# Optimization experiments

Hardware: AMD Instinct MI355X
Metric: run time of the kernel (lower is better)

The kernel has to match this reference:

```python
import jax, jax.numpy as jnp
import numpy as np

N, E = 50000, 400000
HID, HT = 128, 128
HEADS, C = 4, 128  # TransformerConv heads=4, out_channels=hidden_X


def setup_inputs() -> dict:
    key = jax.random.key(0)
    ks = jax.random.split(key, 16)
    s = lambda k, shape, fan: jax.random.normal(k, shape, jnp.float32) / np.sqrt(fan)
    return {
        "edge_index": jax.random.randint(ks[0], (2, E), 0, N, dtype=jnp.int32),
        "h_X": jax.random.normal(ks[1], (N, HID), jnp.float32),
        "h_t": jax.random.normal(ks[2], (1, HT), jnp.float32),
        # TransformerConv params: lin_query/key/value: (HID -> HEADS*C), lin_skip: (HID -> C)
        "Wq": s(ks[3], (HID, HEADS * C), HID), "bq": jnp.zeros((HEADS * C,), jnp.float32),
        "Wk": s(ks[4], (HID, HEADS * C), HID), "bk": jnp.zeros((HEADS * C,), jnp.float32),
        "Wv": s(ks[5], (HID, HEADS * C), HID), "bv": jnp.zeros((HEADS * C,), jnp.float32),
        "Wskip": s(ks[6], (HID, C), HID), "bskip": jnp.zeros((C,), jnp.float32),
        # update_X: Linear(HID+HT -> HID), LayerNorm(HID)
        "Wup": s(ks[7], (HID + HT, HID), HID + HT), "bup": jnp.zeros((HID,), jnp.float32),
        "gamma": jnp.ones((HID,), jnp.float32), "beta": jnp.zeros((HID,), jnp.float32),
    }


def transformer_conv(h_X, edge_index, Wq, bq, Wk, bk, Wv, bv, Wskip, bskip):
    n = h_X.shape[0]
    src, dst = edge_index[0], edge_index[1]  # messages flow src -> dst
    q = (h_X @ Wq + bq).reshape(n, HEADS, C)
    k = (h_X @ Wk + bk).reshape(n, HEADS, C)
    v = (h_X @ Wv + bv).reshape(n, HEADS, C)
    # per-edge attention scores [E, H]
    score = jnp.einsum('ehc,ehc->eh', q[dst], k[src]) / np.sqrt(C)
    # segment softmax over incoming edges of each destination node
    m = jax.ops.segment_max(score, dst, num_segments=n)          # [N, H]
    ex = jnp.exp(score - m[dst])                                 # [E, H]
    denom = jax.ops.segment_sum(ex, dst, num_segments=n)        # [N, H]
    alpha = ex / denom[dst]                                      # [E, H]
    agg = jax.ops.segment_sum(alpha[..., None] * v[src], dst, num_segments=n)  # [N, H, C]
    out = agg.mean(axis=1)                                       # concat=False -> mean over heads
    return out + h_X @ Wskip + bskip                             # root_weight=True


def reference(edge_index, h_X, h_t, Wq, bq, Wk, bk, Wv, bv, Wskip, bskip,
              Wup, bup, gamma, beta):
    n = h_X.shape[0]
    h_att = transformer_conv(h_X, edge_index, Wq, bq, Wk, bk, Wv, bv, Wskip, bskip)
    h_t_exp = jnp.broadcast_to(h_t, (n, h_t.shape[1]))
    h = jnp.concatenate([h_att, h_t_exp], axis=1)
    h = jax.nn.relu(h @ Wup + bup)
    # LayerNorm (eps=1e-5); Dropout is identity in eval
    mu = h.mean(axis=-1, keepdims=True)
    var = ((h - mu) ** 2).mean(axis=-1, keepdims=True)
    return (h - mu) / jnp.sqrt(var + 1e-5) * gamma + beta
```

## Files before the change

### kernel.cpp

```cpp
#include <hip/hip_runtime.h>

typedef unsigned short u16;
typedef unsigned int   u32;

#define HID   128
#define HEADS 4
#define CH    128
#define HC    512
#define KVW   1024
#define UT    32

typedef __bf16 bf16x8v __attribute__((ext_vector_type(8)));
typedef float  f32x4v  __attribute__((ext_vector_type(4)));
union FragU { uint4 u; bf16x8v b; };

static __device__ __forceinline__ float bf2f(u16 u) {
  union { u32 u; float f; } x;
  x.u = ((u32)u) << 16;
  return x.f;
}
static __device__ __forceinline__ u16 f2bf(float f) {
  union { float f; u32 u; } x;
  x.f = f;
  u32 r = x.u + 0x7fffu + ((x.u >> 16) & 1u);
  return (u16)(r >> 16);
}

static __device__ __forceinline__ void unpack8(uint4 raw, float* dst) {
  dst[0] = bf2f((u16)(raw.x & 0xffffu));
  dst[1] = bf2f((u16)(raw.x >> 16));
  dst[2] = bf2f((u16)(raw.y & 0xffffu));
  dst[3] = bf2f((u16)(raw.y >> 16));
  dst[4] = bf2f((u16)(raw.z & 0xffffu));
  dst[5] = bf2f((u16)(raw.z >> 16));
  dst[6] = bf2f((u16)(raw.w & 0xffffu));
  dst[7] = bf2f((u16)(raw.w >> 16));
}

__global__ void hist_kernel(const int* dst_idx, int* deg, int E) {
  int e = blockIdx.x * 256 + threadIdx.x;
  if (e < E) atomicAdd(&deg[dst_idx[e]], 1);
}

__global__ void blocksum_kernel(const int* deg, int* bsums, int n) {
  __shared__ int buf[256];
  int i = blockIdx.x * 256 + threadIdx.x;
  int v = 0;
  if (i < n) v = deg[i];
  buf[threadIdx.x] = v;
  __syncthreads();
  for (int off = 128; off > 0; off >>= 1) {
    if (threadIdx.x < off) buf[threadIdx.x] += buf[threadIdx.x + off];
    __syncthreads();
  }
  if (threadIdx.x == 0) bsums[blockIdx.x] = buf[0];
}

__global__ void scanb_kernel(const int* bsums, int* boffs, int nb) {
  __shared__ int buf[256];
  __shared__ int carry_s;
  int tid = threadIdx.x;
  if (tid == 0) carry_s = 0;
  __syncthreads();
  for (int base = 0; base < nb; base += 256) {
    int i = base + tid;
    int v = 0;
    if (i < nb) v = bsums[i];
    buf[tid] = v;
    __syncthreads();
    for (int off = 1; off < 256; off <<= 1) {
      int t = 0;
      if (tid >= off) t = buf[tid - off];
      __syncthreads();
      buf[tid] += t;
      __syncthreads();
    }
    int incl = buf[tid] + carry_s;
    if (i < nb) boffs[i] = incl - v;
    __syncthreads();
    if (tid == 255) carry_s = incl;
    __syncthreads();
  }
}

__global__ void scanfinal_kernel(const int* deg, const int* boffs,
                                 int* row_ptr, int* cursor, int n) {
  __shared__ int buf[256];
  int tid = threadIdx.x;
  int i = blockIdx.x * 256 + tid;
  int v = 0;
  if (i < n) v = deg[i];
  buf[tid] = v;
  __syncthreads();
  for (int off = 1; off < 256; off <<= 1) {
    int t = 0;
    if (tid >= off) t = buf[tid - off];
    __syncthreads();
    buf[tid] += t;
    __syncthreads();
  }
  int incl = buf[tid] + boffs[blockIdx.x];
  if (i < n) {
    row_ptr[i + 1] = incl;
    cursor[i] = incl - v;
  }
  if (i == 0) row_ptr[0] = 0;
}

__global__ void scatter_kernel(const int* src_idx, const int* dst_idx,
                               int* cursor, int* col, int E) {
  int e = blockIdx.x * 256 + threadIdx.x;
  if (e < E) {
    int pos = atomicAdd(&cursor[dst_idx[e]], 1);
    col[pos] = src_idx[e];
  }
}

__global__ void packH_kernel(const float* __restrict__ hX,
                             u16* __restrict__ hpack, int N, int total) {
  int i = blockIdx.x * 256 + threadIdx.x;
  if (i >= total) return;
  int j = i & 7;
  int lane = (i >> 3) & 63;
  int kc = (i >> 9) & 3;
  int ntile = i >> 11;
  int node = ntile * 16 + (lane & 15);
  int k = kc * 32 + (lane >> 4) * 8 + j;
  float v = (node < N) ? hX[(size_t)node * HID + k] : 0.f;
  hpack[i] = f2bf(v);
}

__global__ void packW4_kernel(const float* __restrict__ Wq,
                              const float* __restrict__ Wk,
                              const float* __restrict__ Wv,
                              const float* __restrict__ Wsk,
                              u16* __restrict__ Wp, int total) {
  int i = blockIdx.x * 256 + threadIdx.x;
  if (i >= total) return;
  int j = i & 7;
  int lane = (i >> 3) & 63;
  int kc = (i >> 9) & 3;
  int ct = i >> 11;
  int n = ct * 16 + (lane & 15);
  int k = kc * 32 + (lane >> 4) * 8 + j;
  float w;
  if (n < 512) w = Wq[(size_t)k * HC + n];
  else if (n < 1024) w = Wk[(size_t)k * HC + (n - 512)];
  else if (n < 1536) w = Wv[(size_t)k * HC + (n - 1024)];
  else w = Wsk[(size_t)k * HID + (n - 1536)];
  Wp[i] = f2bf(w);
}

__global__ __launch_bounds__(256) void mfma_proj_kernel(
    const u16* __restrict__ hpack, const u16* __restrict__ Wp,
    const float* __restrict__ bq, const float* __restrict__ bk,
    const float* __restrict__ bv, const float* __restrict__ bsk,
    u16* __restrict__ qb, u16* __restrict__ kvb,
    float* __restrict__ skipf, int N) {
  int t = threadIdx.x;
  int wv = t >> 6;
  int L = t & 63;
  int bx = blockIdx.x;
  int my0 = blockIdx.y * 8;

  FragU Bf[2][4];
  const u16* wb0 = Wp + (size_t)(bx * 8 + wv * 2) * 2048;
#pragma unroll
  for (int cc = 0; cc < 2; ++cc)
#pragma unroll
    for (int kc = 0; kc < 4; ++kc)
      Bf[cc][kc].u = *(const uint4*)(wb0 + cc * 2048 + kc * 512 + L * 8);

  int colq = L & 15;
  int quad = L >> 4;
  u16* outB_[2];
  int stride_[2];
  float bval[2];
  int nl_[2];
  int isF32_[2];
#pragma unroll
  for (int cc = 0; cc < 2; ++cc) {
    int n = (bx * 8 + wv * 2 + cc) * 16 + colq;
    const float* bias;
    if (n < 512) {
      outB_[cc] = qb; bias = bq; nl_[cc] = n; stride_[cc] = HC; isF32_[cc] = 0;
    } else if (n < 1024) {
      outB_[cc] = kvb; bias = bk; nl_[cc] = n - 512; stride_[cc] = KVW;
      isF32_[cc] = 0;
    } else if (n < 1536) {
      outB_[cc] = kvb; bias = bv; nl_[cc] = n - 512; stride_[cc] = KVW;
      isF32_[cc] = 0;
    } else {
      outB_[cc] = (u16*)skipf; bias = bsk; nl_[cc] = n - 1536; stride_[cc] = 0;
      isF32_[cc] = 1;
    }
    bval[cc] = bias[nl_[cc]];
  }

  const u16* ha = hpack + (size_t)my0 * 2048;

  for (int mt = 0; mt < 8; mt += 2) {
    FragU a0[4], a1[4];
#pragma unroll
    for (int kc = 0; kc < 4; ++kc) {
      a0[kc].u = *(const uint4*)(ha + (size_t)mt * 2048 + kc * 512 + L * 8);
      a1[kc].u =
          *(const uint4*)(ha + (size_t)(mt + 1) * 2048 + kc * 512 + L * 8);
    }

    f32x4v ac00 = (f32x4v){0.f, 0.f, 0.f, 0.f};
    f32x4v ac01 = (f32x4v){0.f, 0.f, 0.f, 0.f};
    f32x4v ac10 = (f32x4v){0.f, 0.f, 0.f, 0.f};
    f32x4v ac11 = (f32x4v){0.f, 0.f, 0.f, 0.f};
#pragma unroll
    for (int kc = 0; kc < 4; ++kc) {
      ac00 = __builtin_amdgcn_mfma_f32_16x16x32_bf16(a0[kc].b, Bf[0][kc].b,
                                                     ac00, 0, 0, 0);
      ac01 = __builtin_amdgcn_mfma_f32_16x16x32_bf16(a0[kc].b, Bf[1][kc].b,
                                                     ac01, 0, 0, 0);
      ac10 = __builtin_amdgcn_mfma_f32_16x16x32_bf16(a1[kc].b, Bf[0][kc].b,
                                                     ac10, 0, 0, 0);
      ac11 = __builtin_amdgcn_mfma_f32_16x16x32_bf16(a1[kc].b, Bf[1][kc].b,
                                                     ac11, 0, 0, 0);
    }

#pragma unroll
    for (int half = 0; half < 2; ++half) {
      int nodeBase = (my0 + mt + half) * 16 + quad * 4;
#pragma unroll
      for (int cc = 0; cc < 2; ++cc) {
        const f32x4v& a =
            half ? (cc ? ac11 : ac10) : (cc ? ac01 : ac00);
        if (isF32_[cc]) {
#pragma unroll
          for (int rg = 0; rg < 4; ++rg) {
            int node = nodeBase + rg;
            if (node < N)
              skipf[(size_t)node * HID + nl_[cc]] = a[rg] + bval[cc];
          }
        } else {
          u16* ob = outB_[cc];
          int st = stride_[cc];
#pragma unroll
          for (int rg = 0; rg < 4; ++rg) {
            int node = nodeBase + rg;
            if (node < N)
              ob[(size_t)node * st + nl_[cc]] = f2bf(a[rg] + bval[cc]);
          }
        }
      }
    }
  }
}

__global__ void fused_attn_kernel(const u16* __restrict__ qb,
                                  const u16* __restrict__ kvb,
                                  const int* __restrict__ row_ptr,
                                  const int* __restrict__ col_src,
                                  float* out, int N) {
  int node = blockIdx.x * 4 + (threadIdx.x >> 6);
  if (node >= N) return;
  int lane = threadIdx.x & 63;
  int head = lane >> 4;
  int r = lane & 15;
  int foff = head * CH + r * 8;
  const float sscale = 0.08838834764831845f;

  float qf[8];
  unpack8(*(const uint4*)(qb + (size_t)node * HC + foff), qf);

  float m = -3.402823466e38f;
  float l = 0.f;
  float acc[8];
  for (int j = 0; j < 8; ++j) acc[j] = 0.f;

  int e0 = row_ptr[node];
  int e1 = row_ptr[node + 1];
  int e = e0;

  for (; e + 4 <= e1; e += 4) {
    int s0 = col_src[e];
    int s1 = col_src[e + 1];
    int s2 = col_src[e + 2];
    int s3 = col_src[e + 3];
    const u16* r0p = kvb + (size_t)s0 * KVW + foff;
    const u16* r1p = kvb + (size_t)s1 * KVW + foff;
    const u16* r2p = kvb + (size_t)s2 * KVW + foff;
    const u16* r3p = kvb + (size_t)s3 * KVW + foff;
    uint4 k0 = *(const uint4*)(r0p);
    uint4 k1 = *(const uint4*)(r1p);
    uint4 k2 = *(const uint4*)(r2p);
    uint4 k3 = *(const uint4*)(r3p);
    uint4 v0 = *(const uint4*)(r0p + 512);
    uint4 v1 = *(const uint4*)(r1p + 512);
    uint4 v2 = *(const uint4*)(r2p + 512);
    uint4 v3 = *(const uint4*)(r3p + 512);

    float kf0[8], kf1[8], kf2[8], kf3[8];
    unpack8(k0, kf0);
    unpack8(k1, kf1);
    unpack8(k2, kf2);
    unpack8(k3, kf3);
    float p0 = 0.f, p1 = 0.f, p2 = 0.f, p3 = 0.f;
    for (int j = 0; j < 8; ++j) {
      p0 = fmaf(kf0[j], qf[j], p0);
      p1 = fmaf(kf1[j], qf[j], p1);
      p2 = fmaf(kf2[j], qf[j], p2);
      p3 = fmaf(kf3[j], qf[j], p3);
    }
    p0 += __shfl_xor(p0, 1);
    p1 += __shfl_xor(p1, 1);
    p2 += __shfl_xor(p2, 1);
    p3 += __shfl_xor(p3, 1);
    p0 += __shfl_xor(p0, 2);
    p1 += __shfl_xor(p1, 2);
    p2 += __shfl_xor(p2, 2);
    p3 += __shfl_xor(p3, 2);
    p0 += __shfl_xor(p0, 4);
    p1 += __shfl_xor(p1, 4);
    p2 += __shfl_xor(p2, 4);
    p3 += __shfl_xor(p3, 4);
    p0 += __shfl_xor(p0, 8);
    p1 += __shfl_xor(p1, 8);
    p2 += __shfl_xor(p2, 8);
    p3 += __shfl_xor(p3, 8);
    float sc0 = p0 * sscale;
    float sc1 = p1 * sscale;
    float sc2 = p2 * sscale;
    float sc3 = p3 * sscale;
    float mnew = fmaxf(fmaxf(m, fmaxf(sc0, sc1)), fmaxf(sc2, sc3));
    float so = __expf(m - mnew);
    float pe0 = __expf(sc0 - mnew);
    float pe1 = __expf(sc1 - mnew);
    float pe2 = __expf(sc2 - mnew);
    float pe3 = __expf(sc3 - mnew);
    l = l * so + (pe0 + pe1) + (pe2 + pe3);
    float vf0[8], vf1[8], vf2[8], vf3[8];
    unpack8(v0, vf0);
    unpack8(v1, vf1);
    unpack8(v2, vf2);
    unpack8(v3, vf3);
    for (int j = 0; j < 8; ++j) {
      float add = fmaf(pe0, vf0[j],
                       fmaf(pe1, vf1[j], fmaf(pe2, vf2[j], pe3 * vf3[j])));
      acc[j] = fmaf(acc[j], so, add);
    }
    m = mnew;
  }

  for (; e < e1; ++e) {
    int s0 = col_src[e];
    const u16* r0p = kvb + (size_t)s0 * KVW + foff;
    uint4 k0 = *(const uint4*)(r0p);
    uint4 v0 = *(const uint4*)(r0p + 512);
    float kf0[8];
    unpack8(k0, kf0);
    float p0 = 0.f;
    for (int j = 0; j < 8; ++j) p0 = fmaf(kf0[j], qf[j], p0);
    p0 += __shfl_xor(p0, 1);
    p0 += __shfl_xor(p0, 2);
    p0 += __shfl_xor(p0, 4);
    p0 += __shfl_xor(p0, 8);
    float sc0 = p0 * sscale;
    float mnew = fmaxf(m, sc0);
    float so = __expf(m - mnew);
    float pe0 = __expf(sc0 - mnew);
    l = l * so + pe0;
    float vf0[8];
    unpack8(v0, vf0);
    for (int j = 0; j < 8; ++j) acc[j] = fmaf(acc[j], so, pe0 * vf0[j]);
    m = mnew;
  }

  float inv = 0.f;
  if (l > 0.f) inv = 1.0f / l;
  float val[8];
  for (int j = 0; j < 8; ++j) {
    float x = acc[j] * inv;
    x += __shfl_xor(x, 16);
    x += __shfl_xor(x, 32);
    val[j] = x * 0.25f;
  }

  if (head == 0) {
    float* p = out + (size_t)node * HID + r * 8;
    float4 a = *(const float4*)(p);
    float4 b = *(const float4*)(p + 4);
    a.x += val[0]; a.y += val[1]; a.z += val[2]; a.w += val[3];
    b.x += val[4]; b.y += val[5]; b.z += val[6]; b.w += val[7];
    *(float4*)(p) = a;
    *(float4*)(p + 4) = b;
  }
}

__global__ void cvec_kernel(const float* h_t, const float* Wup,
                            const float* bup, float* cvec) {
  __shared__ float part[4][128];
  int c = threadIdx.x & 127;
  int kc = threadIdx.x >> 7;
  float acc = 0.f;
  for (int k = kc * 32; k < kc * 32 + 32; ++k)
    acc = fmaf(h_t[k], Wup[(size_t)(128 + k) * 128 + c], acc);
  part[kc][c] = acc;
  __syncthreads();
  if (kc == 0)
    cvec[c] = part[0][c] + part[1][c] + part[2][c] + part[3][c] + bup[c];
}

__global__ __launch_bounds__(256) void ATTLayer_19396072308956_kernel(
    float* out, const float* __restrict__ Wup, const float* __restrict__ cvec,
    const float* __restrict__ gamma, const float* __restrict__ beta, int N) {
  __shared__ float Wl[64 * 128];
  __shared__ float Hl[UT * 128];
  int t = threadIdx.x;
  int n0 = blockIdx.x * UT;

  for (int i = t * 4; i < UT * 128; i += 1024) {
    int node = n0 + (i >> 7);
    float4 v;
    if (node < N) {
      v = *(const float4*)(out + (size_t)node * HID + (i & 127));
    } else {
      v.x = 0.f; v.y = 0.f; v.z = 0.f; v.w = 0.f;
    }
    *(float4*)(Hl + i) = v;
  }

  int wv = t >> 6;
  int r = t & 63;
  int c0 = 2 * r;
  float2 cv = *(const float2*)(cvec + c0);
  float a0[8];
  float a1[8];
  for (int j = 0; j < 8; ++j) {
    a0[j] = cv.x;
    a1[j] = cv.y;
  }

  for (int ph = 0; ph < 2; ++ph) {
    __syncthreads();
    for (int i = t * 4; i < 64 * 128; i += 1024) {
      *(float4*)(Wl + i) = *(const float4*)(Wup + (size_t)ph * 64 * 128 + i);
    }
    __syncthreads();
    const float* hbase = Hl + (wv * 8) * 128 + ph * 64;
#pragma unroll 8
    for (int k = 0; k < 64; ++k) {
      float2 w2 = *(const float2*)(Wl + k * 128 + c0);
      for (int j = 0; j < 8; ++j) {
        float h = hbase[j * 128 + k];
        a0[j] = fmaf(h, w2.x, a0[j]);
        a1[j] = fmaf(h, w2.y, a1[j]);
      }
    }
  }

  float2 g = *(const float2*)(gamma + c0);
  float2 b = *(const float2*)(beta + c0);
  for (int j = 0; j < 8; ++j) {
    int node = n0 + wv * 8 + j;
    float r0 = fmaxf(a0[j], 0.f);
    float r1 = fmaxf(a1[j], 0.f);
    float s = r0 + r1;
    for (int msk = 1; msk < 64; msk <<= 1) s += __shfl_xor(s, msk);
    float mean = s * (1.0f / 128.0f);
    float d0 = r0 - mean;
    float d1 = r1 - mean;
    float sq = d0 * d0 + d1 * d1;
    for (int msk = 1; msk < 64; msk <<= 1) sq += __shfl_xor(sq, msk);
    float rstd = rsqrtf(sq * (1.0f / 128.0f) + 1e-5f);
    if (node < N) {
      float2 o;
      o.x = d0 * rstd * g.x + b.x;
      o.y = d1 * rstd * g.y + b.y;
      *(float2*)(out + (size_t)node * HID + c0) = o;
    }
  }
}

extern "C" void kernel_launch(void* const* d_in, const int* in_sizes, int n_in,
                              void* d_out, int out_size, void* d_ws,
                              size_t ws_size, hipStream_t stream) {
  (void)n_in;
  (void)out_size;
  (void)ws_size;

  const int* edge_index = (const int*)d_in[0];
  const float* hX    = (const float*)d_in[1];
  const float* h_t   = (const float*)d_in[2];
  const float* Wq    = (const float*)d_in[3];
  const float* bq    = (const float*)d_in[4];
  const float* Wk    = (const float*)d_in[5];
  const float* bk    = (const float*)d_in[6];
  const float* Wv    = (const float*)d_in[7];
  const float* bv    = (const float*)d_in[8];
  const float* Wskip = (const float*)d_in[9];
  const float* bskip = (const float*)d_in[10];
  const float* Wup   = (const float*)d_in[11];
  const float* bup   = (const float*)d_in[12];
  const float* gamma = (const float*)d_in[13];
  const float* beta  = (const float*)d_in[14];

  const int E = in_sizes[0] / 2;
  const int N = in_sizes[1] / HID;
  const int* src_idx = edge_index;
  const int* dst_idx = edge_index + E;
  const int NB = (N + 255) / 256;
  const int NTILES = (N + 15) / 16;
  const int NTILES8 = ((NTILES + 7) / 8) * 8;

  char* w = (char*)d_ws;
  size_t off = 0;
  float* cvec = (float*)(w + off);
  off += 256 * 4;
  int* deg = (int*)(w + off);
  off += ((size_t)N * 4 + 255) / 256 * 256;
  int* row_ptr = (int*)(w + off);
  off += ((size_t)(N + 1) * 4 + 255) / 256 * 256;
  int* cursor = (int*)(w + off);
  off += ((size_t)N * 4 + 255) / 256 * 256;
  int* bsums = (int*)(w + off);
  off += ((size_t)NB * 4 + 255) / 256 * 256;
  int* boffs = (int*)(w + off);
  off += ((size_t)NB * 4 + 255) / 256 * 256;
  int* col = (int*)(w + off);
  off += ((size_t)E * 4 + 255) / 256 * 256;
  u16* hpack = (u16*)(w + off);
  off += ((size_t)NTILES8 * 2048 * 2 + 255) / 256 * 256;
  u16* Wp = (u16*)(w + off);
  off += ((size_t)128 * 1664 * 2 + 255) / 256 * 256;
  u16* bigA = (u16*)(w + off);
  off += ((size_t)N * HC * 2 + 255) / 256 * 256;
  u16* bigKV = (u16*)(w + off);
  off += ((size_t)N * KVW * 2 + 255) / 256 * 256;

  float* out = (float*)d_out;

  hipMemsetAsync(deg, 0, (size_t)N * 4, stream);
  hist_kernel<<<(E + 255) / 256, 256, 0, stream>>>(dst_idx, deg, E);
  blocksum_kernel<<<NB, 256, 0, stream>>>(deg, bsums, N);
  scanb_kernel<<<1, 256, 0, stream>>>(bsums, boffs, NB);
  scanfinal_kernel<<<NB, 256, 0, stream>>>(deg, boffs, row_ptr, cursor, N);
  scatter_kernel<<<(E + 255) / 256, 256, 0, stream>>>(src_idx, dst_idx, cursor,
                                                      col, E);

  int totH = NTILES8 * 2048;
  packH_kernel<<<(totH + 255) / 256, 256, 0, stream>>>(hX, hpack, N, totH);
  packW4_kernel<<<(128 * 1664 + 255) / 256, 256, 0, stream>>>(
      Wq, Wk, Wv, Wskip, Wp, 128 * 1664);

  cvec_kernel<<<1, 512, 0, stream>>>(h_t, Wup, bup, cvec);

  mfma_proj_kernel<<<dim3(13, NTILES8 / 8), 256, 0, stream>>>(
      hpack, Wp, bq, bk, bv, bskip, bigA, bigKV, out, N);

  fused_attn_kernel<<<(N + 3) / 4, 256, 0, stream>>>(bigA, bigKV, row_ptr,
                                                     col, out, N);

  ATTLayer_19396072308956_kernel<<<(N + UT - 1) / UT, 256, 0, stream>>>(
      out, Wup, cvec, gamma, beta, N);
}
```

Baseline: 390.0 us.

## Fuse update linear, ReLU and LayerNorm into attention kernel epilogue

Removes the separate update/LayerNorm kernel and runs the Wup matmul, ReLU and LayerNorm in the epilogue of the attention kernel. Each wave stages its node's aggregated row in shared memory, then each lane computes two output channels by streaming Wup from global memory. This saves one launch and a write/read round trip of the intermediate rows. In exchange, Wup is no longer reused across 32 nodes through shared memory, so every wave re-reads the 64KB weight from cache. A block barrier is also added after the attention loop, which can stall waves with short neighbor lists.

```diff
diff --git a/kernel.cpp b/kernel.cpp
--- a/kernel.cpp
+++ b/kernel.cpp
@@ -8,7 +8,6 @@
 #define CH    128
 #define HC    512
 #define KVW   1024
-#define UT    32
 
 typedef __bf16 bf16x8v __attribute__((ext_vector_type(8)));
 typedef float  f32x4v  __attribute__((ext_vector_type(4)));
@@ -257,25 +256,34 @@
                                   const u16* __restrict__ kvb,
                                   const int* __restrict__ row_ptr,
                                   const int* __restrict__ col_src,
-                                  float* out, int N) {
-  int node = blockIdx.x * 4 + (threadIdx.x >> 6);
-  if (node >= N) return;
+                                  float* out,
+                                  const float* __restrict__ Wup,
+                                  const float* __restrict__ cvec,
+                                  const float* __restrict__ gamma,
+                                  const float* __restrict__ beta, int N) {
+  __shared__ float Hs[4][128];
+  int wv = threadIdx.x >> 6;
+  int node = blockIdx.x * 4 + wv;
   int lane = threadIdx.x & 63;
   int head = lane >> 4;
   int r = lane & 15;
   int foff = head * CH + r * 8;
   const float sscale = 0.08838834764831845f;
+  bool valid = (node < N);
 
   float qf[8];
-  unpack8(*(const uint4*)(qb + (size_t)node * HC + foff), qf);
+  if (valid) unpack8(*(const uint4*)(qb + (size_t)node * HC + foff), qf);
 
   float m = -3.402823466e38f;
   float l = 0.f;
   float acc[8];
   for (int j = 0; j < 8; ++j) acc[j] = 0.f;
 
-  int e0 = row_ptr[node];
-  int e1 = row_ptr[node + 1];
+  int e0 = 0, e1 = 0;
+  if (valid) {
+    e0 = row_ptr[node];
+    e1 = row_ptr[node + 1];
+  }
   int e = e0;
 
   for (; e + 4 <= e1; e += 4) {
@@ -382,14 +390,50 @@
     val[j] = x * 0.25f;
   }
 
-  if (head == 0) {
-    float* p = out + (size_t)node * HID + r * 8;
-    float4 a = *(const float4*)(p);
-    float4 b = *(const float4*)(p + 4);
-    a.x += val[0]; a.y += val[1]; a.z += val[2]; a.w += val[3];
-    b.x += val[4]; b.y += val[5]; b.z += val[6]; b.w += val[7];
-    *(float4*)(p) = a;
-    *(float4*)(p + 4) = b;
+  if (valid && head == 0) {
+    const float* srow = out + (size_t)node * HID + r * 8;
+    float4 a = *(const float4*)(srow);
+    float4 b = *(const float4*)(srow + 4);
+    float* hd = &Hs[wv][r * 8];
+    hd[0] = a.x + val[0];
+    hd[1] = a.y + val[1];
+    hd[2] = a.z + val[2];
+    hd[3] = a.w + val[3];
+    hd[4] = b.x + val[4];
+    hd[5] = b.y + val[5];
+    hd[6] = b.z + val[6];
+    hd[7] = b.w + val[7];
+  }
+  __syncthreads();
+
+  int c0 = lane * 2;
+  float a0 = cvec[c0];
+  float a1 = cvec[c0 + 1];
+  const float* hrow = Hs[wv];
+#pragma unroll 8
+  for (int k = 0; k < 128; ++k) {
+    float hk = hrow[k];
+    float2 w2 = *(const float2*)(Wup + (size_t)k * HID + c0);
+    a0 = fmaf(hk, w2.x, a0);
+    a1 = fmaf(hk, w2.y, a1);
+  }
+  float r0 = fmaxf(a0, 0.f);
+  float r1 = fmaxf(a1, 0.f);
+  float s = r0 + r1;
+  for (int msk = 1; msk < 64; msk <<= 1) s += __shfl_xor(s, msk);
+  float mean = s * (1.0f / 128.0f);
+  float d0 = r0 - mean;
+  float d1 = r1 - mean;
+  float sq = d0 * d0 + d1 * d1;
+  for (int msk = 1; msk < 64; msk <<= 1) sq += __shfl_xor(sq, msk);
+  float rstd = rsqrtf(sq * (1.0f / 128.0f) + 1e-5f);
+  if (valid) {
+    float2 g = *(const float2*)(gamma + c0);
+    float2 b = *(const float2*)(beta + c0);
+    float2 o;
+    o.x = d0 * rstd * g.x + b.x;
+    o.y = d1 * rstd * g.y + b.y;
+    *(float2*)(out + (size_t)node * HID + c0) = o;
   }
 }
 
@@ -405,77 +449,6 @@
   __syncthreads();
   if (kc == 0)
     cvec[c] = part[0][c] + part[1][c] + part[2][c] + part[3][c] + bup[c];
-}
-
-__global__ __launch_bounds__(256) void ATTLayer_19396072308956_kernel(
-    float* out, const float* __restrict__ Wup, const float* __restrict__ cvec,
-    const float* __restrict__ gamma, const float* __restrict__ beta, int N) {
-  __shared__ float Wl[64 * 128];
-  __shared__ float Hl[UT * 128];
-  int t = threadIdx.x;
-  int n0 = blockIdx.x * UT;
-
-  for (int i = t * 4; i < UT * 128; i += 1024) {
-    int node = n0 + (i >> 7);
-    float4 v;
-    if (node < N) {
-      v = *(const float4*)(out + (size_t)node * HID + (i & 127));
-    } else {
-      v.x = 0.f; v.y = 0.f; v.z = 0.f; v.w = 0.f;
-    }
-    *(float4*)(Hl + i) = v;
-  }
-
-  int wv = t >> 6;
-  int r = t & 63;
-  int c0 = 2 * r;
-  float2 cv = *(const float2*)(cvec + c0);
-  float a0[8];
-  float a1[8];
-  for (int j = 0; j < 8; ++j) {
-    a0[j] = cv.x;
-    a1[j] = cv.y;
-  }
-
-  for (int ph = 0; ph < 2; ++ph) {
-    __syncthreads();
-    for (int i = t * 4; i < 64 * 128; i += 1024) {
-      *(float4*)(Wl + i) = *(const float4*)(Wup + (size_t)ph * 64 * 128 + i);
-    }
-    __syncthreads();
-    const float* hbase = Hl + (wv * 8) * 128 + ph * 64;
-#pragma unroll 8
-    for (int k = 0; k < 64; ++k) {
-      float2 w2 = *(const float2*)(Wl + k * 128 + c0);
-      for (int j = 0; j < 8; ++j) {
-        float h = hbase[j * 128 + k];
-        a0[j] = fmaf(h, w2.x, a0[j]);
-        a1[j] = fmaf(h, w2.y, a1[j]);
-      }
-    }
-  }
-
-  float2 g = *(const float2*)(gamma + c0);
-  float2 b = *(const float2*)(beta + c0);
-  for (int j = 0; j < 8; ++j) {
-    int node = n0 + wv * 8 + j;
-    float r0 = fmaxf(a0[j], 0.f);
-    float r1 = fmaxf(a1[j], 0.f);
-    float s = r0 + r1;
-    for (int msk = 1; msk < 64; msk <<= 1) s += __shfl_xor(s, msk);
-    float mean = s * (1.0f / 128.0f);
-    float d0 = r0 - mean;
-    float d1 = r1 - mean;
-    float sq = d0 * d0 + d1 * d1;
-    for (int msk = 1; msk < 64; msk <<= 1) sq += __shfl_xor(sq, msk);
-    float rstd = rsqrtf(sq * (1.0f / 128.0f) + 1e-5f);
-    if (node < N) {
-      float2 o;
-      o.x = d0 * rstd * g.x + b.x;
-      o.y = d1 * rstd * g.y + b.y;
-      *(float2*)(out + (size_t)node * HID + c0) = o;
-    }
-  }
 }
 
 extern "C" void kernel_launch(void* const* d_in, const int* in_sizes, int n_in,
@@ -554,9 +527,6 @@
   mfma_proj_kernel<<<dim3(13, NTILES8 / 8), 256, 0, stream>>>(
       hpack, Wp, bq, bk, bv, bskip, bigA, bigKV, out, N);
 
-  fused_attn_kernel<<<(N + 3) / 4, 256, 0, stream>>>(bigA, bigKV, row_ptr,
-                                                     col, out, N);
-
-  ATTLayer_19396072308956_kernel<<<(N + UT - 1) / UT, 256, 0, stream>>>(
-      out, Wup, cvec, gamma, beta, N);
-}
+  fused_attn_kernel<<<(N + 3) / 4, 256, 0, stream>>>(
+      bigA, bigKV, row_ptr, col, out, Wup, cvec, gamma, beta, N);
+}
```

Result: slower. 457.2 us (+17.2%).
